# Performance work log

Measured on AMD Instinct MI355X. Metric: run time of the kernel, lower is better.

Reference implementation:

```python
import jax, jax.numpy as jnp
import numpy as np

N_CENTER, N_NEAR, N_STEPK, N_HOPS = 512, 32, 10, 2
FEAT_NAMES = ["xyz_fea", "pmt_fea", "mad_fea", "dim_fea", "nor_fea", "loc_fea", "fea"]


def pairwise_sqdist(x):
    # x: [B,N,C] -> [B,N,N]
    xx = jnp.sum(x * x, axis=-1)
    return xx[:, :, None] + xx[:, None, :] - 2.0 * jnp.einsum('bnc,bmc->bnm', x, x)


def surface_knn(x, n_near, n_stepk, n_hops=N_HOPS):
    # Iterative surface-KNN: build a step-KNN graph with n_stepk neighbors,
    # expand the neighborhood n_hops times (neighbor-of-neighbor union), then
    # pick the n_near nearest points among the reachable candidate set.
    d = pairwise_sqdist(x)                      # [B,N,N]
    B, N, _ = d.shape
    _, nbr = jax.lax.top_k(-d, n_stepk + 1)     # step neighbors (incl. self)
    b_idx = jnp.arange(B)[:, None, None]
    r_idx = jnp.arange(N)[None, :, None]
    adj = jnp.zeros((B, N, N), jnp.bool_).at[b_idx, r_idx, nbr].set(True)
    reach = adj
    adj_f = adj.astype(jnp.float32)
    for _ in range(n_hops):
        reach = (jnp.einsum('bij,bjk->bik', reach.astype(jnp.float32), adj_f) > 0) | adj
    dm = jnp.where(reach, d, jnp.inf)
    _, idx = jax.lax.top_k(-dm, n_near)         # [B,N,n_near], nearest reachable
    return idx


def fps(x, n_center):
    # Farthest point sampling in the C-dim feature space (dim=dim in source).
    B, N, _ = x.shape
    d = pairwise_sqdist(x)
    barange = jnp.arange(B)

    def step(carry, _):
        mind, prev = carry
        mind = jnp.minimum(mind, d[barange, prev])   # [B,N]
        nxt = jnp.argmax(mind, axis=-1).astype(jnp.int32)
        return (mind, nxt), nxt

    init = (jnp.full((B, N), jnp.inf, jnp.float32), jnp.zeros((B,), jnp.int32))
    _, rest = jax.lax.scan(step, init, None, length=n_center - 1)  # [S-1,B]
    idx = jnp.concatenate([jnp.zeros((1, B), jnp.int32), rest], axis=0)
    return idx.T                                   # [B,S]


def branch(center, grouped, wq, bq, wk, bk, wv, bv, w1, b1, w2, b2):
    # center: [B,S,C], grouped: [B,S,K,C]
    C = center.shape[-1]
    q = center @ wq + bq                           # [B,S,C]
    k = grouped @ wk + bk                          # [B,S,K,C]
    v = grouped @ wv + bv
    scores = jnp.einsum('bsc,bskc->bsk', q, k) / jnp.sqrt(jnp.float32(C))
    attn = jax.nn.softmax(scores, axis=-1)
    out = jnp.einsum('bsk,bskc->bsc', attn, v)     # attention pooling -> [B,S,C]
    h = jax.nn.relu(out @ w1 + b1)                 # MLP (C -> Cout -> Cout)
    return jax.nn.relu(h @ w2 + b2)


def setup_inputs() -> dict:
    key = jax.random.key(0)
    ks = jax.random.split(key, 16)
    B, N, C, CO = 8, 2048, 128, 256
    inp = {}
    for i, name in enumerate(FEAT_NAMES):
        inp[name] = jax.random.normal(ks[i], (B, N, C), jnp.float32)
    s = np.float32(1.0 / np.sqrt(C))
    so = np.float32(1.0 / np.sqrt(CO))
    inp['aw_q'] = jax.random.normal(ks[7], (7, C, C), jnp.float32) * s
    inp['ab_q'] = jnp.zeros((7, C), jnp.float32)
    inp['aw_k'] = jax.random.normal(ks[8], (7, C, C), jnp.float32) * s
    inp['ab_k'] = jnp.zeros((7, C), jnp.float32)
    inp['aw_v'] = jax.random.normal(ks[9], (7, C, C), jnp.float32) * s
    inp['ab_v'] = jnp.zeros((7, C), jnp.float32)
    inp['mw1'] = jax.random.normal(ks[10], (7, C, CO), jnp.float32) * s
    inp['mb1'] = jnp.zeros((7, CO), jnp.float32)
    inp['mw2'] = jax.random.normal(ks[11], (7, CO, CO), jnp.float32) * so
    inp['mb2'] = jnp.zeros((7, CO), jnp.float32)
    return inp


def reference(xyz_fea, pmt_fea, mad_fea, dim_fea, nor_fea, loc_fea, fea,
              aw_q, ab_q, aw_k, ab_k, aw_v, ab_v, mw1, mb1, mw2, mb2):
    B = xyz_fea.shape[0]
    feats = jnp.stack([xyz_fea, pmt_fea, mad_fea, dim_fea, nor_fea, loc_fea, fea], 0)  # [7,B,N,C]
    idx_all = surface_knn(xyz_fea, N_NEAR, N_STEPK)      # [B,N,K]
    fps_idx = fps(xyz_fea, N_CENTER)                     # [B,S]
    b2 = jnp.arange(B)[:, None]                          # [B,1]
    b3 = jnp.arange(B)[:, None, None]                    # [B,1,1]
    centers = feats[:, b2, fps_idx]                      # [7,B,S,C]
    idx = idx_all[b2, fps_idx]                           # [B,S,K]
    grouped = feats[:, b3, idx]                          # [7,B,S,K,C]
    outs = jax.vmap(branch)(centers, grouped, aw_q, ab_q, aw_k, ab_k,
                            aw_v, ab_v, mw1, mb1, mw2, mb2)  # [7,B,S,CO]
    return tuple(outs[i] for i in range(7))
```

## Files before the change

kernel.cpp:

```cpp
#include <hip/hip_runtime.h>
#include <hip/hip_bf16.h>
#include <math.h>

constexpr int BATCH = 8;
constexpr int NPTS  = 2048;
constexpr int CH    = 128;
constexpr int CHO   = 256;
constexpr int NCEN  = 512;
constexpr int NNEI  = 32;
constexpr int NTOP  = 11;
constexpr int NW    = 64;

struct Ptr7 { const float* p[7]; };

__global__ __launch_bounds__(256) void xx_kernel(const float* __restrict__ x,
                                                 float* __restrict__ xx) {
    int p = blockIdx.x * 256 + threadIdx.x;
    if (p >= BATCH * NPTS) return;
    const float4* xr = (const float4*)(x + (size_t)p * CH);
    float s = 0.f;
#pragma unroll
    for (int i = 0; i < CH / 4; i++) {
        float4 v = xr[i];
        s += v.x * v.x + v.y * v.y + v.z * v.z + v.w * v.w;
    }
    xx[p] = s;
}

__global__ __launch_bounds__(256) void dmat_kernel(const float* __restrict__ x,
                                                   const float* __restrict__ xx,
                                                   float* __restrict__ D) {
    __shared__ float As[32][68];
    __shared__ float Bs[32][68];
    int bz = blockIdx.z;
    int i0 = blockIdx.y * 64, j0 = blockIdx.x * 64;
    const float* X = x + (size_t)bz * NPTS * CH;
    int t = threadIdx.x, tx = t & 15, ty = t >> 4;
    int lr = t >> 3, lc = (t & 7) * 4;
    const float* ai0 = X + (size_t)(i0 + lr) * CH;
    const float* ai1 = X + (size_t)(i0 + lr + 32) * CH;
    const float* bj0 = X + (size_t)(j0 + lr) * CH;
    const float* bj1 = X + (size_t)(j0 + lr + 32) * CH;
    float acc[4][4] = {};
    for (int kc = 0; kc < CH; kc += 32) {
        float4 a0 = *(const float4*)(ai0 + kc + lc);
        float4 a1 = *(const float4*)(ai1 + kc + lc);
        float4 b0 = *(const float4*)(bj0 + kc + lc);
        float4 b1 = *(const float4*)(bj1 + kc + lc);
        __syncthreads();
        As[lc + 0][lr] = a0.x; As[lc + 1][lr] = a0.y; As[lc + 2][lr] = a0.z; As[lc + 3][lr] = a0.w;
        As[lc + 0][lr + 32] = a1.x; As[lc + 1][lr + 32] = a1.y; As[lc + 2][lr + 32] = a1.z; As[lc + 3][lr + 32] = a1.w;
        Bs[lc + 0][lr] = b0.x; Bs[lc + 1][lr] = b0.y; Bs[lc + 2][lr] = b0.z; Bs[lc + 3][lr] = b0.w;
        Bs[lc + 0][lr + 32] = b1.x; Bs[lc + 1][lr + 32] = b1.y; Bs[lc + 2][lr + 32] = b1.z; Bs[lc + 3][lr + 32] = b1.w;
        __syncthreads();
#pragma unroll
        for (int kk = 0; kk < 32; kk++) {
            float4 av = *(const float4*)&As[kk][ty * 4];
            float4 bv = *(const float4*)&Bs[kk][tx * 4];
            float a[4] = {av.x, av.y, av.z, av.w};
            float b[4] = {bv.x, bv.y, bv.z, bv.w};
#pragma unroll
            for (int i = 0; i < 4; i++)
#pragma unroll
                for (int j = 0; j < 4; j++) acc[i][j] += a[i] * b[j];
        }
    }
    const float* xxb = xx + bz * NPTS;
    float xi[4], xj[4];
#pragma unroll
    for (int i = 0; i < 4; i++) xi[i] = xxb[i0 + ty * 4 + i];
#pragma unroll
    for (int j = 0; j < 4; j++) xj[j] = xxb[j0 + tx * 4 + j];
#pragma unroll
    for (int i = 0; i < 4; i++) {
        float4 o;
        o.x = xi[i] + xj[0] - 2.f * acc[i][0];
        o.y = xi[i] + xj[1] - 2.f * acc[i][1];
        o.z = xi[i] + xj[2] - 2.f * acc[i][2];
        o.w = xi[i] + xj[3] - 2.f * acc[i][3];
        *(float4*)(D + ((size_t)bz * NPTS + i0 + ty * 4 + i) * NPTS + j0 + tx * 4) = o;
    }
}

__global__ __launch_bounds__(256) void top11_kernel(const float* __restrict__ D,
                                                    unsigned int* __restrict__ adj) {
    __shared__ float row[NPTS];
    __shared__ float rv[256];
    __shared__ int ri[256];
    __shared__ int picks[NTOP + 1];
    int rid = blockIdx.x;
    const float* Dr = D + (size_t)rid * NPTS;
    int t = threadIdx.x;
    float4* rp = (float4*)row;
    rp[t] = ((const float4*)Dr)[t];
    rp[t + 256] = ((const float4*)Dr)[t + 256];
    __syncthreads();
    for (int it = 0; it < NTOP; it++) {
        float bv = row[t];
        int bi = t;
#pragma unroll
        for (int k = 1; k < 8; k++) {
            int j = t + (k << 8);
            float v = row[j];
            if (v < bv) { bv = v; bi = j; }
        }
        rv[t] = bv; ri[t] = bi;
        __syncthreads();
        for (int off = 128; off > 0; off >>= 1) {
            if (t < off) {
                float ov = rv[t + off]; int oi = ri[t + off];
                if (ov < rv[t] || (ov == rv[t] && oi < ri[t])) { rv[t] = ov; ri[t] = oi; }
            }
            __syncthreads();
        }
        if (t == 0) { picks[it] = ri[0]; row[ri[0]] = INFINITY; }
        __syncthreads();
    }
    if (t < NW) {
        unsigned w = 0;
#pragma unroll
        for (int p = 0; p < NTOP; p++) {
            int j = picks[p];
            if ((j >> 5) == t) w |= 1u << (j & 31);
        }
        adj[(size_t)rid * NW + t] = w;
    }
}

__global__ __launch_bounds__(64) void fps_kernel(const float* __restrict__ D,
                                                 int* __restrict__ fps_idx) {
    int b = blockIdx.x, lane = threadIdx.x;
    float mind[32];
#pragma unroll
    for (int r = 0; r < 32; r++) mind[r] = INFINITY;
    int prev = 0;
    if (lane == 0) fps_idx[b * NCEN] = 0;
    const float* Db = D + (size_t)b * NPTS * NPTS;
    for (int s = 1; s < NCEN; s++) {
        const float4* rowp = (const float4*)(Db + (size_t)prev * NPTS);
        float bv = -INFINITY; int bj = NPTS;
#pragma unroll
        for (int k = 0; k < 8; k++) {
            float4 v = rowp[lane + 64 * k];
            int j0 = 4 * (lane + 64 * k);
            float m0 = fminf(mind[4 * k + 0], v.x); mind[4 * k + 0] = m0;
            float m1 = fminf(mind[4 * k + 1], v.y); mind[4 * k + 1] = m1;
            float m2 = fminf(mind[4 * k + 2], v.z); mind[4 * k + 2] = m2;
            float m3 = fminf(mind[4 * k + 3], v.w); mind[4 * k + 3] = m3;
            if (m0 > bv) { bv = m0; bj = j0 + 0; }
            if (m1 > bv) { bv = m1; bj = j0 + 1; }
            if (m2 > bv) { bv = m2; bj = j0 + 2; }
            if (m3 > bv) { bv = m3; bj = j0 + 3; }
        }
#pragma unroll
        for (int off = 32; off > 0; off >>= 1) {
            float ov = __shfl_xor(bv, off);
            int oj = __shfl_xor(bj, off);
            if (ov > bv || (ov == bv && oj < bj)) { bv = ov; bj = oj; }
        }
        if (lane == 0) fps_idx[b * NCEN + s] = bj;
        prev = bj;
    }
}

__global__ void make_gather(const int* __restrict__ fps_idx, int* __restrict__ gatherC) {
    int r = blockIdx.x * 256 + threadIdx.x;
    if (r >= BATCH * NCEN) return;
    int b = r >> 9, s = r & 511;
    gatherC[r] = b * NPTS + fps_idx[b * NCEN + s];
}

__global__ __launch_bounds__(256) void reach_top32_kernel(const unsigned int* __restrict__ adj,
                                                          const float* __restrict__ D,
                                                          const int* __restrict__ fps_idx,
                                                          int* __restrict__ idx_sel) {
    __shared__ unsigned adjw[NW], R1[NW], R2[NW];
    __shared__ int lst[NPTS];
    __shared__ float dst[NPTS];
    __shared__ int cnt;
    __shared__ float rv[256];
    __shared__ int rj[256], rp[256];
    __shared__ int sel[NNEI];
    int s = blockIdx.x, b = blockIdx.y, t = threadIdx.x;
    int i = fps_idx[b * NCEN + s];
    const unsigned* arow = adj + ((size_t)(b * NPTS + i)) * NW;
    if (t < NW) { adjw[t] = arow[t]; R1[t] = arow[t]; }
    if (t == 0) cnt = 0;
    __syncthreads();
    if (t < NW) {
        unsigned w = adjw[t];
        while (w) { int bb = __ffs(w) - 1; w &= w - 1; int p = atomicAdd(&cnt, 1); lst[p] = t * 32 + bb; }
    }
    __syncthreads();
    int n1 = cnt;
    {
        int g = t >> 6, lane = t & 63;
        for (int p = g; p < n1; p += 4) {
            unsigned aw = adj[((size_t)(b * NPTS + lst[p])) * NW + lane];
            atomicOr(&R1[lane], aw);
        }
    }
    __syncthreads();
    if (t == 0) cnt = 0;
    __syncthreads();
    if (t < NW) {
        unsigned w = R1[t];
        while (w) { int bb = __ffs(w) - 1; w &= w - 1; int p = atomicAdd(&cnt, 1); lst[p] = t * 32 + bb; }
        R2[t] = adjw[t];
    }
    __syncthreads();
    int n2 = cnt;
    {
        int g = t >> 6, lane = t & 63;
        for (int p = g; p < n2; p += 4) {
            unsigned aw = adj[((size_t)(b * NPTS + lst[p])) * NW + lane];
            atomicOr(&R2[lane], aw);
        }
    }
    __syncthreads();
    if (t == 0) cnt = 0;
    __syncthreads();
    const float* Dr = D + (size_t)(b * NPTS + i) * NPTS;
    if (t < NW) {
        unsigned w = R2[t];
        while (w) {
            int bb = __ffs(w) - 1; w &= w - 1;
            int j = t * 32 + bb;
            int p = atomicAdd(&cnt, 1);
            lst[p] = j; dst[p] = Dr[j];
        }
    }
    __syncthreads();
    int L = cnt;
    int nsel = L < NNEI ? L : NNEI;
    for (int r = 0; r < nsel; r++) {
        float bv = INFINITY; int bj = 0x7fffffff, bp = -1;
        for (int p = t; p < L; p += 256) {
            float v = dst[p]; int j = lst[p];
            if (v < bv || (v == bv && j < bj)) { bv = v; bj = j; bp = p; }
        }
        rv[t] = bv; rj[t] = bj; rp[t] = bp;
        __syncthreads();
        for (int off = 128; off > 0; off >>= 1) {
            if (t < off) {
                if (rv[t + off] < rv[t] || (rv[t + off] == rv[t] && rj[t + off] < rj[t])) {
                    rv[t] = rv[t + off]; rj[t] = rj[t + off]; rp[t] = rp[t + off];
                }
            }
            __syncthreads();
        }
        if (t == 0) { sel[r] = rj[0]; dst[rp[0]] = INFINITY; }
        __syncthreads();
    }
    if (t == 0 && nsel < NNEI) {
        int r = nsel;
        for (int j = 0; j < NPTS && r < NNEI; j++)
            if (!((R2[j >> 5] >> (j & 31)) & 1)) sel[r++] = j;
    }
    __syncthreads();
    if (t < NNEI) idx_sel[((size_t)(b * NCEN + s)) * NNEI + t] = sel[t];
}

template <int KSIZE, bool RELU>
__device__ __forceinline__ void gemm_tile64(const float* __restrict__ A, int lda,
                                            const int* __restrict__ gather,
                                            const float* __restrict__ W, int ldw,
                                            const float* __restrict__ bias,
                                            float* __restrict__ Out, int ldo) {
    __shared__ float As[32][68];
    __shared__ float Ws[32][68];
    int t = threadIdx.x;
    int tx = t & 15, ty = t >> 4;
    int lr = t >> 3, lc = (t & 7) * 4;
    const float* ar0 = A + (size_t)(gather ? gather[lr] : lr) * lda;
    const float* ar1 = A + (size_t)(gather ? gather[lr + 32] : lr + 32) * lda;
    float acc[4][4] = {};
    for (int kc = 0; kc < KSIZE; kc += 32) {
        float4 a0 = *(const float4*)(ar0 + kc + lc);
        float4 a1 = *(const float4*)(ar1 + kc + lc);
        float4 w0 = *(const float4*)(W + (size_t)(kc + lr) * ldw + lc);
        float4 w1 = *(const float4*)(W + (size_t)(kc + lr) * ldw + lc + 32);
        __syncthreads();
        As[lc + 0][lr] = a0.x; As[lc + 1][lr] = a0.y; As[lc + 2][lr] = a0.z; As[lc + 3][lr] = a0.w;
        As[lc + 0][lr + 32] = a1.x; As[lc + 1][lr + 32] = a1.y; As[lc + 2][lr + 32] = a1.z; As[lc + 3][lr + 32] = a1.w;
        *(float4*)&Ws[lr][lc] = w0;
        *(float4*)&Ws[lr][lc + 32] = w1;
        __syncthreads();
#pragma unroll
        for (int kk = 0; kk < 32; kk++) {
            float4 av = *(const float4*)&As[kk][ty * 4];
            float4 wv = *(const float4*)&Ws[kk][tx * 4];
            float a[4] = {av.x, av.y, av.z, av.w};
            float w[4] = {wv.x, wv.y, wv.z, wv.w};
#pragma unroll
            for (int i = 0; i < 4; i++)
#pragma unroll
                for (int j = 0; j < 4; j++) acc[i][j] += a[i] * w[j];
        }
    }
#pragma unroll
    for (int i = 0; i < 4; i++) {
        int r = ty * 4 + i;
        float4 o;
        o.x = acc[i][0] + bias[tx * 4 + 0];
        o.y = acc[i][1] + bias[tx * 4 + 1];
        o.z = acc[i][2] + bias[tx * 4 + 2];
        o.w = acc[i][3] + bias[tx * 4 + 3];
        if (RELU) {
            o.x = fmaxf(o.x, 0.f); o.y = fmaxf(o.y, 0.f);
            o.z = fmaxf(o.z, 0.f); o.w = fmaxf(o.w, 0.f);
        }
        *(float4*)(Out + (size_t)r * ldo + tx * 4) = o;
    }
}

__global__ __launch_bounds__(256) void kvproj_kernel(Ptr7 feats, const float* __restrict__ awk,
                                                     const float* __restrict__ abk,
                                                     const float* __restrict__ awv,
                                                     const float* __restrict__ abv,
                                                     float* __restrict__ ktab,
                                                     float* __restrict__ vtab) {
    int v = blockIdx.z, ct = blockIdx.y, rt = blockIdx.x;
    bool isv = ct >= 2;
    int c2 = ct & 1;
    const float* A = feats.p[v] + (size_t)rt * 64 * CH;
    const float* W = (isv ? awv : awk) + (size_t)v * CH * CH + c2 * 64;
    const float* bias = (isv ? abv : abk) + v * CH + c2 * 64;
    float* Out = (isv ? vtab : ktab) + (size_t)v * (BATCH * NPTS) * CH + (size_t)rt * 64 * CH + c2 * 64;
    gemm_tile64<CH, false>(A, CH, nullptr, W, CH, bias, Out, CH);
}

__global__ __launch_bounds__(256) void qproj_kernel(Ptr7 feats, const float* __restrict__ awq,
                                                    const float* __restrict__ abq,
                                                    const int* __restrict__ gatherC,
                                                    float* __restrict__ qtab) {
    int v = blockIdx.z, ct = blockIdx.y, rt = blockIdx.x;
    gemm_tile64<CH, false>(feats.p[v], CH, gatherC + rt * 64,
                           awq + (size_t)v * CH * CH + ct * 64, CH,
                           abq + v * CH + ct * 64,
                           qtab + ((size_t)v * (BATCH * NCEN) + rt * 64) * CH + ct * 64, CH);
}

__global__ __launch_bounds__(256) void mlp1_kernel(const float* __restrict__ otab,
                                                   const float* __restrict__ mw1,
                                                   const float* __restrict__ mb1,
                                                   float* __restrict__ htab) {
    int v = blockIdx.z, ct = blockIdx.y, rt = blockIdx.x;
    gemm_tile64<CH, true>(otab + ((size_t)v * (BATCH * NCEN) + rt * 64) * CH, CH, nullptr,
                          mw1 + (size_t)v * CH * CHO + ct * 64, CHO,
                          mb1 + v * CHO + ct * 64,
                          htab + ((size_t)v * (BATCH * NCEN) + rt * 64) * CHO + ct * 64, CHO);
}

__global__ __launch_bounds__(256) void mlp2_kernel(const float* __restrict__ htab,
                                                   const float* __restrict__ mw2,
                                                   const float* __restrict__ mb2,
                                                   float* __restrict__ out) {
    int v = blockIdx.z, ct = blockIdx.y, rt = blockIdx.x;
    gemm_tile64<CHO, true>(htab + ((size_t)v * (BATCH * NCEN) + rt * 64) * CHO, CHO, nullptr,
                           mw2 + (size_t)v * CHO * CHO + ct * 64, CHO,
                           mb2 + v * CHO + ct * 64,
                           out + ((size_t)v * (BATCH * NCEN) + rt * 64) * CHO + ct * 64, CHO);
}

__global__ __launch_bounds__(256) void attn_kernel(const float* __restrict__ qtab,
                                                   const float* __restrict__ ktab,
                                                   const float* __restrict__ vtab,
                                                   const int* __restrict__ idx_sel,
                                                   float* __restrict__ otab) {
    __shared__ float q_s[4][CH];
    __shared__ float attn_s[4][NNEI];
    __shared__ int jj_s[4][NNEI];
    int v = blockIdx.y;
    int t = threadIdx.x, w = t >> 6, lane = t & 63;
    int cg = blockIdx.x * 4 + w;
    int b = cg >> 9, s = cg & 511;
    const float* qr = qtab + ((size_t)v * (BATCH * NCEN) + cg) * CH;
    *(float2*)&q_s[w][lane * 2] = *(const float2*)(qr + lane * 2);
    if (lane < NNEI) jj_s[w][lane] = idx_sel[((size_t)(b * NCEN + s)) * NNEI + lane];
    __syncthreads();
    if (lane < NNEI) {
        int j = jj_s[w][lane];
        const float* kr = ktab + ((size_t)v * (BATCH * NPTS) + b * NPTS + j) * CH;
        float acc = 0.f;
#pragma unroll
        for (int c4 = 0; c4 < CH / 4; c4++) {
            float4 qv = *(const float4*)&q_s[w][c4 * 4];
            float4 kv = *(const float4*)(kr + c4 * 4);
            acc += qv.x * kv.x + qv.y * kv.y + qv.z * kv.z + qv.w * kv.w;
        }
        float sc = acc * 0.08838834764831845f;
        float m = sc;
#pragma unroll
        for (int off = 16; off > 0; off >>= 1) m = fmaxf(m, __shfl_xor(m, off, 32));
        float e = expf(sc - m);
        float sum = e;
#pragma unroll
        for (int off = 16; off > 0; off >>= 1) sum += __shfl_xor(sum, off, 32);
        attn_s[w][lane] = e / sum;
    }
    __syncthreads();
    float2 o = {0.f, 0.f};
    const float* vbase = vtab + ((size_t)v * (BATCH * NPTS) + b * NPTS) * CH;
    for (int tt = 0; tt < NNEI; tt++) {
        int j = jj_s[w][tt];
        float a = attn_s[w][tt];
        float2 vv = *(const float2*)(vbase + (size_t)j * CH + lane * 2);
        o.x += a * vv.x;
        o.y += a * vv.y;
    }
    *(float2*)(otab + ((size_t)v * (BATCH * NCEN) + cg) * CH + lane * 2) = o;
}

extern "C" void kernel_launch(void* const* d_in, const int* in_sizes, int n_in,
                              void* d_out, int out_size, void* d_ws, size_t ws_size,
                              hipStream_t stream) {
    (void)in_sizes; (void)n_in; (void)out_size;
    Ptr7 feats;
    for (int i = 0; i < 7; i++) feats.p[i] = (const float*)d_in[i];
    const float* awq = (const float*)d_in[7];
    const float* abq = (const float*)d_in[8];
    const float* awk = (const float*)d_in[9];
    const float* abk = (const float*)d_in[10];
    const float* awv = (const float*)d_in[11];
    const float* abv = (const float*)d_in[12];
    const float* mw1 = (const float*)d_in[13];
    const float* mb1 = (const float*)d_in[14];
    const float* mw2 = (const float*)d_in[15];
    const float* mb2 = (const float*)d_in[16];
    const float* xyz = feats.p[0];

    char* ws = (char*)d_ws;
    size_t SZ_D = (size_t)BATCH * NPTS * NPTS * 4;
    float* D = (float*)ws;
    float* ktab = (float*)ws;
    float* vtab = (float*)(ws + (size_t)7 * BATCH * NPTS * CH * 4);
    size_t off = SZ_D;
    float* xx = (float*)(ws + off); off += (size_t)BATCH * NPTS * 4;
    unsigned* adjb = (unsigned*)(ws + off); off += (size_t)BATCH * NPTS * NW * 4;
    int* fpsidx = (int*)(ws + off); off += (size_t)BATCH * NCEN * 4;
    int* idxsel = (int*)(ws + off); off += (size_t)BATCH * NCEN * NNEI * 4;
    int* gatherC = (int*)(ws + off); off += (size_t)BATCH * NCEN * 4;
    float* qtab = (float*)(ws + off); off += (size_t)7 * BATCH * NCEN * CH * 4;
    float* otab = (float*)(ws + off); off += (size_t)7 * BATCH * NCEN * CH * 4;
    float* htab = (float*)(ws + off); off += (size_t)7 * BATCH * NCEN * CHO * 4;
    if (ws_size < off) return;

    xx_kernel<<<dim3((BATCH * NPTS + 255) / 256), dim3(256), 0, stream>>>(xyz, xx);
    dmat_kernel<<<dim3(NPTS / 64, NPTS / 64, BATCH), dim3(256), 0, stream>>>(xyz, xx, D);
    top11_kernel<<<dim3(BATCH * NPTS), dim3(256), 0, stream>>>(D, adjb);
    fps_kernel<<<dim3(BATCH), dim3(64), 0, stream>>>(D, fpsidx);
    make_gather<<<dim3((BATCH * NCEN + 255) / 256), dim3(256), 0, stream>>>(fpsidx, gatherC);
    reach_top32_kernel<<<dim3(NCEN, BATCH), dim3(256), 0, stream>>>(adjb, D, fpsidx, idxsel);
    kvproj_kernel<<<dim3(BATCH * NPTS / 64, 4, 7), dim3(256), 0, stream>>>(feats, awk, abk, awv, abv, ktab, vtab);
    qproj_kernel<<<dim3(BATCH * NCEN / 64, 2, 7), dim3(256), 0, stream>>>(feats, awq, abq, gatherC, qtab);
    attn_kernel<<<dim3(BATCH * NCEN / 4, 7), dim3(256), 0, stream>>>(qtab, ktab, vtab, idxsel, otab);
    mlp1_kernel<<<dim3(BATCH * NCEN / 64, 4, 7), dim3(256), 0, stream>>>(otab, mw1, mb1, htab);
    mlp2_kernel<<<dim3(BATCH * NCEN / 64, 4, 7), dim3(256), 0, stream>>>(htab, mw2, mb2, (float*)d_out);
}
```

Baseline: 1.277 ms.

## Fuse FPS into top-11 kernel so serial FPS overlaps KNN blocks

Merges the single-wave-per-batch FPS loop into the top-11 adjacency kernel. The first BATCH blocks run FPS while the remaining blocks do per-row top-11 selection, so the long serial FPS chain overlaps the parallel KNN work instead of running after it. It also hoists all eight row loads ahead of the min/argmax chain to raise memory-level parallelism. The FPS blocks now launch with 256 threads and retire three waves immediately, and the kernel's resource use is set by the larger branch.

```diff
diff --git a/kernel.cpp b/kernel.cpp
--- a/kernel.cpp
+++ b/kernel.cpp
@@ -82,13 +82,59 @@
     }
 }
 
-__global__ __launch_bounds__(256) void top11_kernel(const float* __restrict__ D,
-                                                    unsigned int* __restrict__ adj) {
+__global__ __launch_bounds__(256) void knn_fps_kernel(const float* __restrict__ D,
+                                                      unsigned int* __restrict__ adj,
+                                                      int* __restrict__ fps_idx) {
+    if (blockIdx.x < BATCH) {
+        int lane = threadIdx.x;
+        if (lane >= 64) return;
+        int b = blockIdx.x;
+        float mind[32];
+#pragma unroll
+        for (int r = 0; r < 32; r++) mind[r] = INFINITY;
+        int prev = 0;
+        if (lane == 0) fps_idx[b * NCEN] = 0;
+        const float* Db = D + (size_t)b * NPTS * NPTS;
+        for (int s = 1; s < NCEN; s++) {
+            const float4* rowp = (const float4*)(Db + (size_t)prev * NPTS);
+            float4 v0 = rowp[lane + 0 * 64];
+            float4 v1 = rowp[lane + 1 * 64];
+            float4 v2 = rowp[lane + 2 * 64];
+            float4 v3 = rowp[lane + 3 * 64];
+            float4 v4 = rowp[lane + 4 * 64];
+            float4 v5 = rowp[lane + 5 * 64];
+            float4 v6 = rowp[lane + 6 * 64];
+            float4 v7 = rowp[lane + 7 * 64];
+            float bv = -INFINITY; int bj = NPTS;
+            float4 vv[8] = {v0, v1, v2, v3, v4, v5, v6, v7};
+#pragma unroll
+            for (int k = 0; k < 8; k++) {
+                int j0 = 4 * (lane + 64 * k);
+                float m0 = fminf(mind[4 * k + 0], vv[k].x); mind[4 * k + 0] = m0;
+                float m1 = fminf(mind[4 * k + 1], vv[k].y); mind[4 * k + 1] = m1;
+                float m2 = fminf(mind[4 * k + 2], vv[k].z); mind[4 * k + 2] = m2;
+                float m3 = fminf(mind[4 * k + 3], vv[k].w); mind[4 * k + 3] = m3;
+                if (m0 > bv) { bv = m0; bj = j0 + 0; }
+                if (m1 > bv) { bv = m1; bj = j0 + 1; }
+                if (m2 > bv) { bv = m2; bj = j0 + 2; }
+                if (m3 > bv) { bv = m3; bj = j0 + 3; }
+            }
+#pragma unroll
+            for (int off = 32; off > 0; off >>= 1) {
+                float ov = __shfl_xor(bv, off);
+                int oj = __shfl_xor(bj, off);
+                if (ov > bv || (ov == bv && oj < bj)) { bv = ov; bj = oj; }
+            }
+            if (lane == 0) fps_idx[b * NCEN + s] = bj;
+            prev = bj;
+        }
+        return;
+    }
     __shared__ float row[NPTS];
     __shared__ float rv[256];
     __shared__ int ri[256];
     __shared__ int picks[NTOP + 1];
-    int rid = blockIdx.x;
+    int rid = blockIdx.x - BATCH;
     const float* Dr = D + (size_t)rid * NPTS;
     int t = threadIdx.x;
     float4* rp = (float4*)row;
@@ -124,42 +170,6 @@
             if ((j >> 5) == t) w |= 1u << (j & 31);
         }
         adj[(size_t)rid * NW + t] = w;
-    }
-}
-
-__global__ __launch_bounds__(64) void fps_kernel(const float* __restrict__ D,
-                                                 int* __restrict__ fps_idx) {
-    int b = blockIdx.x, lane = threadIdx.x;
-    float mind[32];
-#pragma unroll
-    for (int r = 0; r < 32; r++) mind[r] = INFINITY;
-    int prev = 0;
-    if (lane == 0) fps_idx[b * NCEN] = 0;
-    const float* Db = D + (size_t)b * NPTS * NPTS;
-    for (int s = 1; s < NCEN; s++) {
-        const float4* rowp = (const float4*)(Db + (size_t)prev * NPTS);
-        float bv = -INFINITY; int bj = NPTS;
-#pragma unroll
-        for (int k = 0; k < 8; k++) {
-            float4 v = rowp[lane + 64 * k];
-            int j0 = 4 * (lane + 64 * k);
-            float m0 = fminf(mind[4 * k + 0], v.x); mind[4 * k + 0] = m0;
-            float m1 = fminf(mind[4 * k + 1], v.y); mind[4 * k + 1] = m1;
-            float m2 = fminf(mind[4 * k + 2], v.z); mind[4 * k + 2] = m2;
-            float m3 = fminf(mind[4 * k + 3], v.w); mind[4 * k + 3] = m3;
-            if (m0 > bv) { bv = m0; bj = j0 + 0; }
-            if (m1 > bv) { bv = m1; bj = j0 + 1; }
-            if (m2 > bv) { bv = m2; bj = j0 + 2; }
-            if (m3 > bv) { bv = m3; bj = j0 + 3; }
-        }
-#pragma unroll
-        for (int off = 32; off > 0; off >>= 1) {
-            float ov = __shfl_xor(bv, off);
-            int oj = __shfl_xor(bj, off);
-            if (ov > bv || (ov == bv && oj < bj)) { bv = ov; bj = oj; }
-        }
-        if (lane == 0) fps_idx[b * NCEN + s] = bj;
-        prev = bj;
     }
 }
 
@@ -448,8 +458,7 @@
 
     xx_kernel<<<dim3((BATCH * NPTS + 255) / 256), dim3(256), 0, stream>>>(xyz, xx);
     dmat_kernel<<<dim3(NPTS / 64, NPTS / 64, BATCH), dim3(256), 0, stream>>>(xyz, xx, D);
-    top11_kernel<<<dim3(BATCH * NPTS), dim3(256), 0, stream>>>(D, adjb);
-    fps_kernel<<<dim3(BATCH), dim3(64), 0, stream>>>(D, fpsidx);
+    knn_fps_kernel<<<dim3(BATCH + BATCH * NPTS), dim3(256), 0, stream>>>(D, adjb, fpsidx);
     make_gather<<<dim3((BATCH * NCEN + 255) / 256), dim3(256), 0, stream>>>(fpsidx, gatherC);
     reach_top32_kernel<<<dim3(NCEN, BATCH), dim3(256), 0, stream>>>(adjb, D, fpsidx, idxsel);
     kvproj_kernel<<<dim3(BATCH * NPTS / 64, 4, 7), dim3(256), 0, stream>>>(feats, awk, abk, awv, abv, ktab, vtab);
```

New measurement: 1.162 ms. 9.0% less time.
